# Performance work log

Hardware: AMD Instinct MI355X
Metric: run time of the kernel (lower is better)

Reference implementation:

```python
import jax, jax.numpy as jnp
import numpy as np

# constants from VMD_block.__init__ (K=4, alpha=2000, tau=0, DC=0, init=1, tol=5e-5, max_N=5)
K = 4
ALPHA = 2000.0
TAU = 0.0
TOL = 5e-05
MAX_N = 5


def _mvmd(f):
    """Multivariate VMD (Rehman & Aftab 2019) on f: (C, T) real signals.
    Returns modes u: (K, C, T). Shared center frequencies omega across channels."""
    C, T = f.shape
    half = T // 2
    T2 = 2 * T
    # mirror extension to length 2T
    fM = jnp.concatenate([f[:, :half][:, ::-1], f, f[:, half:][:, ::-1]], axis=1)
    freqs = (jnp.arange(1, T2 + 1, dtype=f.dtype) / T2) - 0.5 - (1.0 / T2)  # (T2,)
    f_hat = jnp.fft.fftshift(jnp.fft.fft(fM, axis=1), axes=1).astype(jnp.complex64)
    h2 = T2 // 2
    f_hat_plus = f_hat.at[:, :h2].set(0.0)  # keep analytic (positive-freq) part
    fpos = freqs[h2:]

    omega0 = (0.5 / K) * jnp.arange(K, dtype=f.dtype)  # init == 1, DC == 0
    u0 = jnp.zeros((K, C, T2), dtype=jnp.complex64)
    lam0 = jnp.zeros((C, T2), dtype=jnp.complex64)

    def cond(st):
        _, _, _, n, uDiff = st
        return jnp.logical_and(uDiff > TOL, n < MAX_N)

    def body(st):
        u, omega, lam, n, _ = st
        u_prev = u
        sum_all = jnp.sum(u, axis=0)  # (C, T2)
        for k in range(K):  # Gauss-Seidel mode updates; K is small & static
            sum_uk = sum_all - u[k]
            denom = 1.0 + ALPHA * (freqs - omega[k]) ** 2  # (T2,)
            u_k = (f_hat_plus - sum_uk - lam / 2.0) / denom
            sum_all = sum_uk + u_k
            u = u.at[k].set(u_k)
            power = jnp.abs(u_k[:, h2:]) ** 2  # (C, T2/2) positive freqs
            omega = omega.at[k].set(jnp.sum(fpos * power) / jnp.sum(power))
        lam = lam + TAU * (sum_all - f_hat_plus)  # tau == 0 -> dual ascent is a no-op
        d = u - u_prev
        uDiff = jnp.abs(jnp.sum(d * jnp.conj(d)) / T2) + jnp.finfo(jnp.float32).eps
        return u, omega, lam, n + 1, uDiff.astype(jnp.float32)

    st0 = (u0, omega0, lam0, jnp.int32(0), jnp.float32(TOL + 1.0))
    u, omega, lam, n, uDiff = jax.lax.while_loop(cond, body, st0)

    # rebuild full spectrum via Hermitian symmetry, back to time domain
    u_hat = jnp.zeros((K, C, T2), dtype=jnp.complex64)
    u_hat = u_hat.at[:, :, h2:].set(u[:, :, h2:])
    u_hat = u_hat.at[:, :, 1:h2 + 1].set(jnp.conj(u[:, :, h2:])[:, :, ::-1])
    u_hat = u_hat.at[:, :, 0].set(jnp.conj(u_hat[:, :, -1]))
    ut = jnp.real(jnp.fft.ifft(jnp.fft.ifftshift(u_hat, axes=-1), axis=-1))
    return ut[:, :, T2 // 4: 3 * T2 // 4]  # crop mirror padding -> (K, C, T)


def setup_inputs() -> dict:
    key = jax.random.key(0)
    x = jax.random.normal(key, (8, 2048, 64), dtype=jnp.float32)  # (B, T, C)
    return {"x": x}


def reference(x):
    B, T, C = x.shape
    xr = jnp.transpose(x, (0, 2, 1)).reshape(B * C, T)  # (B*C, T)
    u = _mvmd(xr)  # (K, B*C, T)
    x_l = jnp.transpose(u[0].reshape(B, C, T), (0, 2, 1))  # lowest-freq mode -> (B, T, C)
    x_h = x - x_l
    return (x_h, x_l)
```

## Files before the change

### kernel.cpp

```cpp
#include <hip/hip_runtime.h>
#include <math.h>

#define TLEN 2048
#define T2   4096
#define H2   2048
#define NBLK 512
#define EPS32 1.1920928955078125e-07

__device__ __forceinline__ double ld_acc(const double* p){
  return __hip_atomic_load(p, __ATOMIC_RELAXED, __HIP_MEMORY_SCOPE_AGENT);
}

__device__ __forceinline__ void gbar(unsigned* bar){
  __syncthreads();
  if (threadIdx.x == 0){
    __hip_atomic_fetch_add(bar, 1u, __ATOMIC_RELAXED, __HIP_MEMORY_SCOPE_AGENT);
    unsigned spins = 0;
    while (__hip_atomic_load(bar, __ATOMIC_RELAXED, __HIP_MEMORY_SCOPE_AGENT) < NBLK){
      if (++spins > (1u << 21)) break;
      __builtin_amdgcn_s_sleep(2);
    }
  }
  __syncthreads();
}

#define R2REG(ZA, ZB, W, SGN, E, O) {                           \
  float wy_ = (SGN) * W.y;                                      \
  E = make_float2(ZA.x + ZB.x, ZA.y + ZB.y);                    \
  float dx_ = ZA.x - ZB.x, dy_ = ZA.y - ZB.y;                   \
  O = make_float2(dx_ * W.x - dy_ * wy_, dx_ * wy_ + dy_ * W.x); }

#define R4REG(A, B, C, D, W1, W2, W3, SGN, Y0, Y1, Y2, Y3) {    \
  float w1y_ = (SGN)*W1.y, w2y_ = (SGN)*W2.y, w3y_ = (SGN)*W3.y;\
  float t0x = A.x + C.x, t0y = A.y + C.y;                       \
  float t1x = A.x - C.x, t1y = A.y - C.y;                       \
  float t2x = B.x + D.x, t2y = B.y + D.y;                       \
  float t3x = (SGN) * (B.y - D.y), t3y = -(SGN) * (B.x - D.x);  \
  Y0 = make_float2(t0x + t2x, t0y + t2y);                       \
  float y1x = t1x + t3x, y1y = t1y + t3y;                       \
  float y2x = t0x - t2x, y2y = t0y - t2y;                       \
  float y3x = t1x - t3x, y3y = t1y - t3y;                       \
  Y1 = make_float2(y1x*W1.x - y1y*w1y_, y1x*w1y_ + y1y*W1.x);   \
  Y2 = make_float2(y2x*W2.x - y2y*w2y_, y2x*w2y_ + y2y*W2.x);   \
  Y3 = make_float2(y3x*W3.x - y3y*w3y_, y3x*w3y_ + y3y*W3.x); }

__device__ __forceinline__ void fused2(float2 z0, float2 z1, float2 z2, float2 z3,
                                       float2 z4, float2 z5, float2 z6, float2 z7,
                                       const float2* twl, float sgn, float2* dst){
  const int tid = threadIdx.x;
  float2 wa = twl[2*tid], wb = twl[2*tid+512], wc = twl[2*tid+1024], wd = twl[2*tid+1536];
  float2 e0,o0,e1,o1,e2,o2,e3,o3;
  R2REG(z0, z4, wa, sgn, e0, o0)
  R2REG(z1, z5, wb, sgn, e1, o1)
  R2REG(z2, z6, wc, sgn, e2, o2)
  R2REG(z3, z7, wd, sgn, e3, o3)
  float2 w1 = twl[4*tid], w2 = twl[8*tid], w3 = twl[12*tid];
  float2 a0,a1,a2,a3, b0,b1,b2,b3;
  R4REG(e0, e1, e2, e3, w1, w2, w3, sgn, a0, a1, a2, a3)
  R4REG(o0, o1, o2, o3, w1, w2, w3, sgn, b0, b1, b2, b3)
  float4* d4 = reinterpret_cast<float4*>(dst + 8 * tid);
  d4[0] = make_float4(a0.x, a0.y, b0.x, b0.y);
  d4[1] = make_float4(a1.x, a1.y, b1.x, b1.y);
  d4[2] = make_float4(a2.x, a2.y, b2.x, b2.y);
  d4[3] = make_float4(a3.x, a3.y, b3.x, b3.y);
}

__device__ __forceinline__ void r4_stages(float2* src, float2* dst,
                                          const float2* twl, float sgn,
                                          int first, int cnt){
  const int tid = threadIdx.x;
  #pragma unroll 1
  for (int t = 0; t < cnt; ++t){
    const int L = 2 << (2 * (first + t));
    const int Lm = L - 1;
    #pragma unroll
    for (int bf = 0; bf < 2; ++bf){
      int idx = tid + (bf << 8);
      int q  = idx & Lm;
      int tb = idx - q;
      float2 a = src[idx];
      float2 b = src[idx + 512];
      float2 c = src[idx + 1024];
      float2 d = src[idx + 1536];
      float2 w1 = twl[2 * tb];
      float2 w2 = twl[4 * tb];
      float2 w3 = twl[6 * tb];
      float2 y0, y1, y2, y3;
      R4REG(a, b, c, d, w1, w2, w3, sgn, y0, y1, y2, y3)
      int ob = q + (tb << 2);
      dst[ob]         = y0;
      dst[ob + L]     = y1;
      dst[ob + 2 * L] = y2;
      dst[ob + 3 * L] = y3;
    }
    __syncthreads();
    float2* tt = src; src = dst; dst = tt;
  }
}

__device__ __forceinline__ float wredf(float v){
  #pragma unroll
  for (int off = 32; off; off >>= 1) v += __shfl_down(v, off);
  return v;
}

__device__ __forceinline__ void red9(float a0, float a1, float a2, float a3,
                                     float a4, float a5, float a6, float a7,
                                     float a8, float* redf, double* accs){
  const int tid = threadIdx.x, wave = tid >> 6, lane = tid & 63;
  float r;
  r = wredf(a0); if (lane == 0) redf[ 0 + wave] = r;
  r = wredf(a1); if (lane == 0) redf[ 4 + wave] = r;
  r = wredf(a2); if (lane == 0) redf[ 8 + wave] = r;
  r = wredf(a3); if (lane == 0) redf[12 + wave] = r;
  r = wredf(a4); if (lane == 0) redf[16 + wave] = r;
  r = wredf(a5); if (lane == 0) redf[20 + wave] = r;
  r = wredf(a6); if (lane == 0) redf[24 + wave] = r;
  r = wredf(a7); if (lane == 0) redf[28 + wave] = r;
  r = wredf(a8); if (lane == 0) redf[32 + wave] = r;
  __syncthreads();
  if (tid < 9){
    double s = (double)redf[tid*4+0] + (double)redf[tid*4+1]
             + (double)redf[tid*4+2] + (double)redf[tid*4+3];
    atomicAdd(&accs[tid], s);
  }
}

#define MODE_S(UXc, UYc, OMc, AFP, AP) {                       \
  float ox_ = sx - (UXc), oy_ = sy - (UYc);                    \
  float d_  = fj - (OMc);                                      \
  float den_ = 1.0f + 2000.0f * d_ * d_;                       \
  float nx_ = (Fx - ox_) / den_, ny_ = (Fy - oy_) / den_;      \
  float pw_ = nx_ * nx_ + ny_ * ny_;                           \
  AFP += fj * pw_;  AP += pw_;                                 \
  float ddx_ = nx_ - (UXc), ddy_ = ny_ - (UYc);                \
  aD += ddx_ * ddx_ + ddy_ * ddy_;                             \
  (UXc) = nx_; (UYc) = ny_;                                    \
  sx = ox_ + nx_; sy = oy_ + ny_; }

#define BIN_S(PP, FV, UX, UY) {                                \
  float Fx = FV.x, Fy = FV.y;                                  \
  float fj = (float)(tid + ((PP) << 8)) * (1.0f / 4096.0f);    \
  float sx = UX.x + UX.y + UX.z + UX.w;                        \
  float sy = UY.x + UY.y + UY.z + UY.w;                        \
  MODE_S(UX.x, UY.x, om.x, aFP0, aP0)                          \
  MODE_S(UX.y, UY.y, om.y, aFP1, aP1)                          \
  MODE_S(UX.z, UY.z, om.z, aFP2, aP2)                          \
  MODE_S(UX.w, UY.w, om.w, aFP3, aP3) }

#define IT1(PP, FV, UX, UY) { UX = make_float4(0.f,0.f,0.f,0.f); \
                              UY = make_float4(0.f,0.f,0.f,0.f); \
                              BIN_S(PP, FV, UX, UY) }

#define FCOMP(PP, FV) {                                        \
  int k = tid + ((PP) << 8);                                   \
  float2 A  = bufA[k];                                         \
  float2 Zm = bufA[(2048 - k) & 2047];                         \
  float px = 0.5f * (A.x + Zm.x), py = 0.5f * (A.y - Zm.y);    \
  float qx = 0.5f * (A.x - Zm.x), qy = 0.5f * (A.y + Zm.y);    \
  float2 W = twl[k];                                           \
  FV = make_float2(px + W.x * qy + W.y * qx,                   \
                   py - W.x * qx + W.y * qy); }

#define HERMU(PP, FV, UX, UY) {                                \
  int j = tid + ((PP) << 8);                                   \
  float vx, vy;                                                \
  if (act){                                                    \
    float sx = UX.y + UX.z + UX.w;                             \
    float sy = UY.y + UY.z + UY.w;                             \
    float fj = (float)j * (1.0f / 4096.0f);                    \
    float dd = fj - om0;                                       \
    float den = 1.0f + 2000.0f * dd * dd;                      \
    vx = (FV.x - sx) / den; vy = (FV.y - sy) / den;            \
  } else { vx = UX.x; vy = UY.x; }                             \
  bufA[j] = make_float2(vx, vy); }

#define ZPCOMP(PP, ZV) {                                       \
  int k = tid + ((PP) << 8);                                   \
  if (k == 0){                                                 \
    float e = bufA[0].x + bufA[2047].x;                        \
    float o = bufA[0].x - bufA[2047].x;                        \
    ZV = make_float2(e, o);                                    \
  } else {                                                     \
    float2 A  = bufA[k];                                       \
    float2 Bm = bufA[2048 - k];                                \
    float ex = A.x + Bm.x, ey = A.y - Bm.y;                    \
    float dx = A.x - Bm.x, dy = A.y + Bm.y;                    \
    float2 W = twl[k];                                         \
    float ox = dx * W.x + dy * W.y;                            \
    float oy = dy * W.x - dx * W.y;                            \
    ZV = make_float2(ex - oy, ey + ox);                        \
  } }

#define FOR8F(M) M(0,f0,ux0,uy0) M(1,f1,ux1,uy1) M(2,f2,ux2,uy2) M(3,f3,ux3,uy3) \
                 M(4,f4,ux4,uy4) M(5,f5,ux5,uy5) M(6,f6,ux6,uy6) M(7,f7,ux7,uy7)

#define ILAST(IDX, Y1, Y2) {                                   \
  float2 a = bufA[IDX];                                        \
  float2 bb = bufA[(IDX) + 512];                               \
  float2 c = bufA[(IDX) + 1024];                               \
  float2 d = bufA[(IDX) + 1536];                               \
  float t1x = a.x - c.x, t1y = a.y - c.y;                      \
  float t3x = -(bb.y - d.y), t3y = (bb.x - d.x);               \
  Y1 = make_float2(t1x + t3x, t1y + t3y);                      \
  float t0x = a.x + c.x, t0y = a.y + c.y;                      \
  float t2x = bb.x + d.x, t2y = bb.y + d.y;                    \
  Y2 = make_float2(t0x - t2x, t0y - t2y); }

__global__ void __attribute__((amdgpu_flat_work_group_size(256, 256),
                               amdgpu_waves_per_eu(2, 2)))
k_main(const float* __restrict__ x, unsigned* __restrict__ bar,
       double* __restrict__ accs, float* __restrict__ xh, float* __restrict__ xl){
  __shared__ float2 twl[3072];
  __shared__ float2 bufA[H2];
  __shared__ float2 bufB[H2];
  __shared__ float redf[36];
  __shared__ float somf[8];
  const int tid = threadIdx.x;
  const int b = blockIdx.x & 7, ch = blockIdx.x >> 3;
  const float* xc = x + (size_t)b * TLEN * 64 + ch;

  #pragma unroll
  for (int i = 0; i < 12; ++i){
    int p = tid + (i << 8);
    float ang = (float)(-1.5339807878856412e-3 * (double)p);
    float s, c;
    sincosf(ang, &s, &c);
    twl[p] = make_float2(c, s);
  }

  float2 z0, z1, z2, z3, z4, z5, z6, z7;
  z0 = make_float2(xc[(size_t)(1023 - 2*tid) * 64], xc[(size_t)(1022 - 2*tid) * 64]);
  z1 = make_float2(xc[(size_t)( 511 - 2*tid) * 64], xc[(size_t)( 510 - 2*tid) * 64]);
  { int t = 2*tid;        z2 = make_float2(xc[(size_t)t*64], xc[(size_t)(t+1)*64]); }
  { int t = 2*tid + 512;  z3 = make_float2(xc[(size_t)t*64], xc[(size_t)(t+1)*64]); }
  { int t = 2*tid + 1024; z4 = make_float2(xc[(size_t)t*64], xc[(size_t)(t+1)*64]); }
  { int t = 2*tid + 1536; z5 = make_float2(xc[(size_t)t*64], xc[(size_t)(t+1)*64]); }
  z6 = make_float2(xc[(size_t)(2047 - 2*tid) * 64], xc[(size_t)(2046 - 2*tid) * 64]);
  z7 = make_float2(xc[(size_t)(1535 - 2*tid) * 64], xc[(size_t)(1534 - 2*tid) * 64]);
  __syncthreads();

  fused2(z0, z1, z2, z3, z4, z5, z6, z7, twl, 1.0f, bufA);
  __syncthreads();
  r4_stages(bufA, bufB, twl, 1.0f, 1, 4);

  float2 f0, f1, f2, f3, f4, f5, f6, f7;
  FCOMP(0, f0) FCOMP(1, f1) FCOMP(2, f2) FCOMP(3, f3)
  FCOMP(4, f4) FCOMP(5, f5) FCOMP(6, f6) FCOMP(7, f7)

  float4 ux0, ux1, ux2, ux3, ux4, ux5, ux6, ux7;
  float4 uy0, uy1, uy2, uy3, uy4, uy5, uy6, uy7;
  float4 om = make_float4(0.0f, 0.125f, 0.25f, 0.375f);

  {
    float aFP0=0,aFP1=0,aFP2=0,aFP3=0,aP0=0,aP1=0,aP2=0,aP3=0,aD=0;
    FOR8F(IT1)
    red9(aFP0,aFP1,aFP2,aFP3,aP0,aP1,aP2,aP3,aD, redf, accs);
  }

  bool active = true;
  double* slot = accs;
  #pragma unroll 1
  for (int it = 0; it < 3; ++it){
    gbar(bar + it);
    if (tid < 4) somf[tid] = (float)(ld_acc(slot + tid) / ld_acc(slot + 4 + tid));
    if (tid == 7) somf[7] = (ld_acc(slot + 8) * (1.0/4096.0) + EPS32 > 5e-5) ? 1.f : 0.f;
    __syncthreads();
    if (active){
      if (somf[7] != 0.0f){
        om.x = somf[0]; om.y = somf[1]; om.z = somf[2]; om.w = somf[3];
      } else active = false;
    }
    if (active){
      float aFP0=0,aFP1=0,aFP2=0,aFP3=0,aP0=0,aP1=0,aP2=0,aP3=0,aD=0;
      FOR8F(BIN_S)
      red9(aFP0,aFP1,aFP2,aFP3,aP0,aP1,aP2,aP3,aD, redf, slot + 9);
    }
    slot += 9;
  }
  gbar(bar + 3);
  if (tid == 0) somf[0] = (float)(ld_acc(slot) / ld_acc(slot + 4));
  if (tid == 7) somf[7] = (ld_acc(slot + 8) * (1.0/4096.0) + EPS32 > 5e-5) ? 1.f : 0.f;
  __syncthreads();

  {
    bool act = active && (somf[7] != 0.0f);
    float om0 = somf[0];
    FOR8F(HERMU)
    __syncthreads();
    float2 p0, p1, p2, p3, p4, p5, p6, p7;
    ZPCOMP(0, p0) ZPCOMP(1, p1) ZPCOMP(2, p2) ZPCOMP(3, p3)
    ZPCOMP(4, p4) ZPCOMP(5, p5) ZPCOMP(6, p6) ZPCOMP(7, p7)
    __syncthreads();
    fused2(p0, p1, p2, p3, p4, p5, p6, p7, twl, -1.0f, bufB);
    __syncthreads();
    r4_stages(bufB, bufA, twl, -1.0f, 1, 3);
  }

  {
    const float scale = 1.0f / 4096.0f;
    float2 y1a, y2a, y1b, y2b;
    ILAST(tid,       y1a, y2a)
    ILAST(tid + 256, y1b, y2b)
    #define STOUT(YV, T0, ZS) {                                \
      size_t o0 = ((size_t)(b * TLEN + (T0))) * 64 + ch;       \
      float l0 = YV.x * scale, l1 = YV.y * scale;              \
      xh[o0]      = ZS.x - l0;  xl[o0]      = l0;              \
      xh[o0 + 64] = ZS.y - l1;  xl[o0 + 64] = l1; }
    STOUT(y1a, 2*tid,        z2)
    STOUT(y1b, 2*tid + 512,  z3)
    STOUT(y2a, 2*tid + 1024, z4)
    STOUT(y2b, 2*tid + 1536, z5)
  }
}

extern "C" void kernel_launch(void* const* d_in, const int* in_sizes, int n_in,
                              void* d_out, int out_size, void* d_ws, size_t ws_size,
                              hipStream_t stream){
  const float* x = (const float*)d_in[0];
  float* out_xh = (float*)d_out;
  float* out_xl = out_xh + (size_t)8 * TLEN * 64;

  char* ws = (char*)d_ws;
  unsigned* bar = (unsigned*)ws;
  double* accs  = (double*)(ws + 128);

  hipMemsetAsync(ws, 0, 512, stream);
  k_main<<<NBLK, 256, 0, stream>>>(x, bar, accs, out_xh, out_xl);
}
```

Before: 133.0 us.

## Replace flat grid barrier with tree-combined barrier broadcasting omega record

```diff
diff --git a/kernel.cpp b/kernel.cpp
--- a/kernel.cpp
+++ b/kernel.cpp
@@ -10,18 +10,44 @@
 __device__ __forceinline__ double ld_acc(const double* p){
   return __hip_atomic_load(p, __ATOMIC_RELAXED, __HIP_MEMORY_SCOPE_AGENT);
 }
-
-__device__ __forceinline__ void gbar(unsigned* bar){
-  __syncthreads();
-  if (threadIdx.x == 0){
-    __hip_atomic_fetch_add(bar, 1u, __ATOMIC_RELAXED, __HIP_MEMORY_SCOPE_AGENT);
-    unsigned spins = 0;
-    while (__hip_atomic_load(bar, __ATOMIC_RELAXED, __HIP_MEMORY_SCOPE_AGENT) < NBLK){
-      if (++spins > (1u << 21)) break;
-      __builtin_amdgcn_s_sleep(2);
+__device__ __forceinline__ unsigned ld_u32(const unsigned* p){
+  return __hip_atomic_load(p, __ATOMIC_RELAXED, __HIP_MEMORY_SCOPE_AGENT);
+}
+__device__ __forceinline__ void st_u32(unsigned* p, unsigned v){
+  __hip_atomic_store(p, v, __ATOMIC_RELAXED, __HIP_MEMORY_SCOPE_AGENT);
+}
+
+__device__ void tree_sync_omega(unsigned* leaf, unsigned* root, unsigned* rec,
+                                const double* slot, float* somf, int gid){
+  unsigned old = __hip_atomic_fetch_add(leaf + (size_t)gid * 32, 1u,
+                                        __ATOMIC_RELAXED, __HIP_MEMORY_SCOPE_AGENT);
+  if (old == 63u){
+    unsigned oldr = __hip_atomic_fetch_add(root, 1u,
+                                           __ATOMIC_RELAXED, __HIP_MEMORY_SCOPE_AGENT);
+    if (oldr == 7u){
+      double uD = ld_acc(slot + 8);
+      float o0 = (float)(ld_acc(slot + 0) / ld_acc(slot + 4));
+      float o1 = (float)(ld_acc(slot + 1) / ld_acc(slot + 5));
+      float o2 = (float)(ld_acc(slot + 2) / ld_acc(slot + 6));
+      float o3 = (float)(ld_acc(slot + 3) / ld_acc(slot + 7));
+      unsigned fl = (uD * (1.0 / 4096.0) + EPS32 > 5e-5) ? 3u : 1u;
+      st_u32(rec + 1, __float_as_uint(o0));
+      st_u32(rec + 2, __float_as_uint(o1));
+      st_u32(rec + 3, __float_as_uint(o2));
+      st_u32(rec + 4, __float_as_uint(o3));
+      __hip_atomic_store(rec, fl, __ATOMIC_RELEASE, __HIP_MEMORY_SCOPE_AGENT);
     }
   }
-  __syncthreads();
+  unsigned f, spins = 0;
+  while (((f = ld_u32(rec)) & 1u) == 0u){
+    if (++spins > (1u << 22)) break;
+    __builtin_amdgcn_s_sleep(2);
+  }
+  somf[7] = (f & 2u) ? 1.f : 0.f;
+  somf[0] = __uint_as_float(ld_u32(rec + 1));
+  somf[1] = __uint_as_float(ld_u32(rec + 2));
+  somf[2] = __uint_as_float(ld_u32(rec + 3));
+  somf[3] = __uint_as_float(ld_u32(rec + 4));
 }
 
 #define R2REG(ZA, ZB, W, SGN, E, O) {                           \
@@ -209,7 +235,8 @@
 
 __global__ void __attribute__((amdgpu_flat_work_group_size(256, 256),
                                amdgpu_waves_per_eu(2, 2)))
-k_main(const float* __restrict__ x, unsigned* __restrict__ bar,
+k_main(const float* __restrict__ x, unsigned* __restrict__ leaf,
+       unsigned* __restrict__ root, unsigned* __restrict__ rec,
        double* __restrict__ accs, float* __restrict__ xh, float* __restrict__ xl){
   __shared__ float2 twl[3072];
   __shared__ float2 bufA[H2];
@@ -218,15 +245,14 @@
   __shared__ float somf[8];
   const int tid = threadIdx.x;
   const int b = blockIdx.x & 7, ch = blockIdx.x >> 3;
+  const int gid = blockIdx.x & 7;
   const float* xc = x + (size_t)b * TLEN * 64 + ch;
 
   #pragma unroll
   for (int i = 0; i < 12; ++i){
     int p = tid + (i << 8);
-    float ang = (float)(-1.5339807878856412e-3 * (double)p);
-    float s, c;
-    sincosf(ang, &s, &c);
-    twl[p] = make_float2(c, s);
+    float rev = (float)p * (-1.0f / 4096.0f);
+    twl[p] = make_float2(__builtin_amdgcn_cosf(rev), __builtin_amdgcn_sinf(rev));
   }
 
   float2 z0, z1, z2, z3, z4, z5, z6, z7;
@@ -259,12 +285,12 @@
   }
 
   bool active = true;
-  double* slot = accs;
   #pragma unroll 1
   for (int it = 0; it < 3; ++it){
-    gbar(bar + it);
-    if (tid < 4) somf[tid] = (float)(ld_acc(slot + tid) / ld_acc(slot + 4 + tid));
-    if (tid == 7) somf[7] = (ld_acc(slot + 8) * (1.0/4096.0) + EPS32 > 5e-5) ? 1.f : 0.f;
+    __syncthreads();
+    if (tid == 0)
+      tree_sync_omega(leaf + it * 256, root + it * 32, rec + it * 32,
+                      accs + it * 16, somf, gid);
     __syncthreads();
     if (active){
       if (somf[7] != 0.0f){
@@ -274,13 +300,13 @@
     if (active){
       float aFP0=0,aFP1=0,aFP2=0,aFP3=0,aP0=0,aP1=0,aP2=0,aP3=0,aD=0;
       FOR8F(BIN_S)
-      red9(aFP0,aFP1,aFP2,aFP3,aP0,aP1,aP2,aP3,aD, redf, slot + 9);
+      red9(aFP0,aFP1,aFP2,aFP3,aP0,aP1,aP2,aP3,aD, redf, accs + (it + 1) * 16);
     }
-    slot += 9;
-  }
-  gbar(bar + 3);
-  if (tid == 0) somf[0] = (float)(ld_acc(slot) / ld_acc(slot + 4));
-  if (tid == 7) somf[7] = (ld_acc(slot + 8) * (1.0/4096.0) + EPS32 > 5e-5) ? 1.f : 0.f;
+  }
+  __syncthreads();
+  if (tid == 0)
+    tree_sync_omega(leaf + 3 * 256, root + 3 * 32, rec + 3 * 32,
+                    accs + 3 * 16, somf, gid);
   __syncthreads();
 
   {
@@ -322,9 +348,11 @@
   float* out_xl = out_xh + (size_t)8 * TLEN * 64;
 
   char* ws = (char*)d_ws;
-  unsigned* bar = (unsigned*)ws;
-  double* accs  = (double*)(ws + 128);
-
-  hipMemsetAsync(ws, 0, 512, stream);
-  k_main<<<NBLK, 256, 0, stream>>>(x, bar, accs, out_xh, out_xl);
-}
+  unsigned* leaf = (unsigned*)ws;
+  unsigned* root = (unsigned*)(ws + 4096);
+  unsigned* rec  = (unsigned*)(ws + 4608);
+  double*   accs = (double*)  (ws + 5120);
+
+  hipMemsetAsync(ws, 0, 5632, stream);
+  k_main<<<NBLK, 256, 0, stream>>>(x, leaf, root, rec, accs, out_xh, out_xl);
+}
```

New measurement: 129.1 us. -2.9%, faster.
